# Optimization experiments

Measured on AMD Instinct MI355X. Metric: run time of the kernel, lower is better.

## Reference

```python
import jax, jax.numpy as jnp
import numpy as np

PI = np.pi
NQ = 9  # qubits: edge 0-2, node 3-6 (center=3, neighbor0=4), anc1=7, anc2=8


def _mlp(x, W1, b1, W2, b2):
    h = jax.nn.leaky_relu(x @ W1 + b1, negative_slope=0.2)
    return h @ W2 + b2


def _ry(t):
    h = 0.5 * t
    c = jnp.cos(h).astype(jnp.complex64)
    s = jnp.sin(h).astype(jnp.complex64)
    return jnp.stack([jnp.stack([c, -s]), jnp.stack([s, c])])


def _rx(t):
    h = 0.5 * t
    c = jnp.cos(h).astype(jnp.complex64)
    s = jnp.sin(h).astype(jnp.complex64)
    return jnp.stack([jnp.stack([c, -1j * s]), jnp.stack([-1j * s, c])])


def _rz(t):
    h = (0.5 * t).astype(jnp.complex64)
    e = jnp.exp(-1j * h)
    z = jnp.zeros((), jnp.complex64)
    return jnp.stack([jnp.stack([e, z]), jnp.stack([z, jnp.conj(e)])])


def _ap1(state, U, q):
    s = jnp.moveaxis(state, q, 0)
    s = jnp.tensordot(U, s, axes=([1], [0]))
    return jnp.moveaxis(s, 0, q)


def _apc(state, U, c, t):  # controlled-U, control c, target t
    s = jnp.moveaxis(state, (c, t), (0, 1))
    s1 = jnp.tensordot(U, s[1], axes=([1], [0]))
    s = jnp.stack([s[0], s1])
    return jnp.moveaxis(s, (0, 1), (c, t))


def _cz(state, a, b):
    s = jnp.moveaxis(state, (a, b), (0, 1))
    s = s.at[1, 1].multiply(-1.0)
    return jnp.moveaxis(s, (0, 1), (a, b))


def _pqc(data, theta):
    # data: [18] per-graphlet angles, theta: [27] shared weights; returns <X_center>
    state = jnp.zeros((2,) * NQ, jnp.complex64).at[(0,) * NQ].set(1.0)
    for i in range(3):  # edge qubits: ry, rz
        state = _ap1(state, _ry(data[2 * i]), i)
        state = _ap1(state, _rz(data[2 * i + 1]), i)
    for i in range(4):  # node qubits: ry, rz
        state = _ap1(state, _ry(data[6 + 2 * i]), 3 + i)
        state = _ap1(state, _rz(data[7 + 2 * i]), 3 + i)
    state = _apc(state, _rx(data[14]), 4, 7)  # neighbor -> anc1, c-rx(phi0)
    state = _apc(state, _ry(data[15]), 0, 7)  # edge0    -> anc1, c-ry(phi1)
    state = _apc(state, _rz(data[16]), 4, 8)  # neighbor -> anc2, c-rz(phi2)
    state = _apc(state, _ry(data[17]), 0, 8)  # edge0    -> anc2, c-ry(phi3)
    for b, qs in enumerate([(0, 4, 7), (7, 4, 8), (3, 7, 8)]):  # A, B, U blocks
        th = theta[9 * b:9 * b + 9]
        for i, q in enumerate(qs):
            state = _ap1(state, _rx(th[3 * i + 0]), q)
            state = _ap1(state, _ry(th[3 * i + 1]), q)
            state = _ap1(state, _rz(th[3 * i + 2]), q)
        state = _cz(state, qs[0], qs[1])
        state = _cz(state, qs[1], qs[2])
        state = _cz(state, qs[2], qs[0])
    xs = jnp.moveaxis(jnp.moveaxis(state, 3, 0)[::-1], 0, 3)  # apply X on qubit 3
    return jnp.real(jnp.vdot(state, xs)).astype(jnp.float32)


def setup_inputs() -> dict:
    N, E, K, G = 6000, 96000, 4, 32
    rng = np.random.default_rng(0)
    src = rng.integers(0, N, E)
    dst = (src + 1 + rng.integers(0, N - 1, E)) % N  # no self loops
    pairs = np.stack([np.minimum(src, dst), np.maximum(src, dst)], 1)
    keymap = {(int(u), int(v)): i for i, (u, v) in enumerate(pairs)}
    und = np.unique(np.concatenate([np.stack([src, dst], 1), np.stack([dst, src], 1)], 0), axis=0)
    deg = np.bincount(und[:, 0], minlength=N)
    starts = np.concatenate([[0], np.cumsum(deg)])[:-1]
    gn = np.full((N, K), -1, np.int32)
    gn[:, 0] = np.arange(N)
    ge = np.full((N, K - 1), -1, np.int32)
    for j in range(K - 1):
        has = deg > j
        cs = np.nonzero(has)[0]
        nb = und[starts[has] + j, 1]
        gn[cs, 1 + j] = nb
        for c, n in zip(cs.tolist(), nb.tolist()):
            ge[c, j] = keymap[(min(c, n), max(c, n))]
    batch = ((np.arange(N) * G) // N).astype(np.int32)
    key = jax.random.key(0)
    ks = jax.random.split(key, 12)

    def dense(k, i, o):
        return jax.random.normal(k, (i, o), jnp.float32) / np.sqrt(i)

    return dict(
        node_feat=jax.random.normal(ks[0], (N, 16), jnp.float32),
        edge_attr=jax.random.normal(ks[1], (E, 8), jnp.float32),
        node_W1=dense(ks[2], 16, 128), node_b1=jnp.zeros((128,), jnp.float32),
        node_W2=dense(ks[3], 128, 2), node_b2=jnp.zeros((2,), jnp.float32),
        edge_W1=dense(ks[4], 8, 128), edge_b1=jnp.zeros((128,), jnp.float32),
        edge_W2=dense(ks[5], 128, 2), edge_b2=jnp.zeros((2,), jnp.float32),
        theta=jax.random.uniform(ks[6], (1, 27), jnp.float32, -0.1, 0.1),
        upd_W1=dense(ks[7], 3, 128)[None], upd_b1=jnp.zeros((1, 128), jnp.float32),
        upd_W2=dense(ks[8], 128, 2)[None], upd_b2=jnp.zeros((1, 2), jnp.float32),
        head_W1=dense(ks[9], 2, 2), head_b1=jnp.zeros((2,), jnp.float32),
        head_W2=dense(ks[10], 2, 2), head_b2=jnp.zeros((2,), jnp.float32),
        graphlet_nodes=jnp.asarray(gn), graphlet_edges=jnp.asarray(ge),
        batch=jnp.asarray(batch), num_graphs=G,
    )


def reference(node_feat, edge_attr, node_W1, node_b1, node_W2, node_b2,
              edge_W1, edge_b1, edge_W2, edge_b2, theta,
              upd_W1, upd_b1, upd_W2, upd_b2,
              head_W1, head_b1, head_W2, head_b2,
              graphlet_nodes, graphlet_edges, batch, num_graphs):
    node_f = jnp.tanh(_mlp(node_feat, node_W1, node_b1, node_W2, node_b2)) * PI
    edge_f = jnp.tanh(_mlp(edge_attr, edge_W1, edge_b1, edge_W2, edge_b2)) * PI
    nm = (graphlet_nodes >= 0).astype(node_f.dtype)[..., None]  # pad mask
    em = (graphlet_edges >= 0).astype(edge_f.dtype)[..., None]
    gn = jnp.clip(graphlet_nodes, 0)
    ge = jnp.clip(graphlet_edges, 0)
    N = node_f.shape[0]
    e_feat = edge_f[ge] * em  # [N,3,2] fixed across hops
    for h in range(theta.shape[0]):
        n_feat = node_f[gn] * nm  # [N,4,2]
        phis = jnp.stack([n_feat[:, 1, 0], e_feat[:, 0, 0], n_feat[:, 1, 1], e_feat[:, 0, 1]], 1)
        data = jnp.concatenate([e_feat.reshape(N, 6), n_feat.reshape(N, 8), phis], 1)  # [N,18]
        exp = jax.vmap(_pqc, in_axes=(0, None))(data, theta[h])  # [N]
        upd_inp = jnp.concatenate([node_f[gn[:, 0]], exp[:, None]], 1)  # [N,3]
        upd = _mlp(upd_inp, upd_W1[h], upd_b1[h], upd_W2[h], upd_b2[h])  # [N,2]
        node_f = node_f + jnp.zeros_like(node_f).at[gn[:, 0]].add(upd)
    seg = jax.ops.segment_sum(node_f, batch, num_segments=num_graphs)
    cnt = jax.ops.segment_sum(jnp.ones((N,), node_f.dtype), batch, num_segments=num_graphs)
    emb = seg / cnt[:, None]  # global mean pool
    return _mlp(emb, head_W1, head_b1, head_W2, head_b2)
```

## Files before the change

kernel.cpp:

```cpp
#include <hip/hip_runtime.h>

#define PI_F 3.14159265358979323846f

struct C2 { float r, i; };
struct M2 { C2 m[2][2]; };

__device__ __forceinline__ C2 cmul(C2 a, C2 b){ return C2{a.r*b.r - a.i*b.i, a.r*b.i + a.i*b.r}; }
__device__ __forceinline__ C2 cadd(C2 a, C2 b){ return C2{a.r+b.r, a.i+b.i}; }

__device__ __forceinline__ M2 mmul(M2 A, M2 B){
  M2 R;
  #pragma unroll
  for (int r=0;r<2;++r)
    #pragma unroll
    for (int c=0;c<2;++c)
      R.m[r][c] = cadd(cmul(A.m[r][0],B.m[0][c]), cmul(A.m[r][1],B.m[1][c]));
  return R;
}
__device__ __forceinline__ M2 m_rx(float t){ float s,c; __sincosf(0.5f*t,&s,&c);
  M2 U; U.m[0][0]=C2{c,0}; U.m[0][1]=C2{0,-s}; U.m[1][0]=C2{0,-s}; U.m[1][1]=C2{c,0}; return U; }
__device__ __forceinline__ M2 m_ry(float t){ float s,c; __sincosf(0.5f*t,&s,&c);
  M2 U; U.m[0][0]=C2{c,0}; U.m[0][1]=C2{-s,0}; U.m[1][0]=C2{s,0}; U.m[1][1]=C2{c,0}; return U; }
__device__ __forceinline__ M2 m_rz(float t){ float s,c; __sincosf(0.5f*t,&s,&c);
  M2 U; U.m[0][0]=C2{c,-s}; U.m[0][1]=C2{0,0}; U.m[1][0]=C2{0,0}; U.m[1][1]=C2{c,s}; return U; }
__device__ __forceinline__ M2 fuse_zyx(float tz, float ty, float tx){ return mmul(m_rz(tz), mmul(m_ry(ty), m_rx(tx))); }

__device__ __forceinline__ float fast_tanh(float x){
  float e = __expf(2.f*x);
  return 1.f - 2.f/(e + 1.f);
}

__device__ __forceinline__ M2 selM(bool c, M2 U){
  M2 E;
  E.m[0][0] = c ? U.m[0][0] : C2{1.f,0.f};
  E.m[0][1] = c ? U.m[0][1] : C2{0.f,0.f};
  E.m[1][0] = c ? U.m[1][0] : C2{0.f,0.f};
  E.m[1][1] = c ? U.m[1][1] : C2{1.f,0.f};
  return E;
}

__device__ __forceinline__ M2 loadM(const float* __restrict__ p){
  M2 U;
  U.m[0][0]=C2{p[0],p[1]}; U.m[0][1]=C2{p[2],p[3]};
  U.m[1][0]=C2{p[4],p[5]}; U.m[1][1]=C2{p[6],p[7]};
  return U;
}


template<int STRIDE>
__device__ __forceinline__ void applyReg(M2 U, float (&sr)[8], float (&si)[8]){
  #pragma unroll
  for (int r0=0;r0<8;++r0){
    if (r0 & STRIDE) continue;
    const int r1 = r0 | STRIDE;
    C2 a0{sr[r0], si[r0]}, a1{sr[r1], si[r1]};
    C2 n0 = cadd(cmul(U.m[0][0],a0), cmul(U.m[0][1],a1));
    C2 n1 = cadd(cmul(U.m[1][0],a0), cmul(U.m[1][1],a1));
    sr[r0]=n0.r; si[r0]=n0.i; sr[r1]=n1.r; si[r1]=n1.i;
  }
}

template<int MASK>
__device__ __forceinline__ void applyLane(M2 U, float (&sr)[8], float (&si)[8], int lane){
  const bool b = (lane & MASK) != 0;
  const C2 cs = b ? U.m[1][1] : U.m[0][0];
  const C2 cp = b ? U.m[1][0] : U.m[0][1];
  #pragma unroll
  for (int j=0;j<8;++j){
    float pr  = __shfl_xor(sr[j], MASK);
    float pim = __shfl_xor(si[j], MASK);
    float nr = cs.r*sr[j] - cs.i*si[j] + cp.r*pr  - cp.i*pim;
    float ni = cs.r*si[j] + cs.i*sr[j] + cp.r*pim + cp.i*pr;
    sr[j]=nr; si[j]=ni;
  }
}

__global__ void features_kernel(const float* __restrict__ node_feat,
                                const float* __restrict__ edge_attr,
                                const int* __restrict__ ge,
                                const float* __restrict__ nW1, const float* __restrict__ nb1,
                                const float* __restrict__ nW2, const float* __restrict__ nb2,
                                const float* __restrict__ eW1, const float* __restrict__ eb1,
                                const float* __restrict__ eW2, const float* __restrict__ eb2,
                                float* __restrict__ node_f, float* __restrict__ ef,
                                int N,
                                const float* __restrict__ theta, float* __restrict__ tm){
  const int row = blockIdx.x*blockDim.x + threadIdx.x;
  if (row < 9){
    M2 U = fuse_zyx(theta[3*row+2], theta[3*row+1], theta[3*row+0]);
    float* p = tm + row*8;
    p[0]=U.m[0][0].r; p[1]=U.m[0][0].i;
    p[2]=U.m[0][1].r; p[3]=U.m[0][1].i;
    p[4]=U.m[1][0].r; p[5]=U.m[1][0].i;
    p[6]=U.m[1][1].r; p[7]=U.m[1][1].i;
  }
  if (row < N){
    float xi[16];
    #pragma unroll
    for (int i=0;i<16;++i) xi[i] = node_feat[row*16+i];
    float a0 = nb2[0], a1 = nb2[1];
    #pragma unroll 4
    for (int j=0;j<128;++j){
      float h = nb1[j];
      #pragma unroll
      for (int i=0;i<16;++i) h = fmaf(xi[i], nW1[i*128+j], h);
      h = h > 0.f ? h : 0.2f*h;
      a0 = fmaf(h, nW2[j*2+0], a0);
      a1 = fmaf(h, nW2[j*2+1], a1);
    }
    node_f[row*2+0] = PI_F * fast_tanh(a0);
    node_f[row*2+1] = PI_F * fast_tanh(a1);
  } else {
    const int r = row - N;
    if (r >= 3*N) return;
    const int e = ge[r];
    if (e < 0){ ef[r*2+0] = 0.f; ef[r*2+1] = 0.f; return; }
    float xi[8];
    #pragma unroll
    for (int i=0;i<8;++i) xi[i] = edge_attr[e*8+i];
    float a0 = eb2[0], a1 = eb2[1];
    #pragma unroll 4
    for (int j=0;j<128;++j){
      float h = eb1[j];
      #pragma unroll
      for (int i=0;i<8;++i) h = fmaf(xi[i], eW1[i*128+j], h);
      h = h > 0.f ? h : 0.2f*h;
      a0 = fmaf(h, eW2[j*2+0], a0);
      a1 = fmaf(h, eW2[j*2+1], a1);
    }
    ef[r*2+0] = PI_F * fast_tanh(a0);
    ef[r*2+1] = PI_F * fast_tanh(a1);
  }
}

__global__ void __launch_bounds__(256)
pqc_kernel(const float* __restrict__ node_f, const float* __restrict__ ef,
           const int* __restrict__ gn,
           const float* __restrict__ tm,
           const float* __restrict__ uW1, const float* __restrict__ ub1,
           const float* __restrict__ uW2, const float* __restrict__ ub2,
           float* __restrict__ upd, int N){
  const int lane = threadIdx.x & 63;
  const int n = blockIdx.x*4 + (threadIdx.x >> 6);
  if (n >= N) return;

  float d[18];
  #pragma unroll
  for (int j=0;j<6;++j) d[j] = ef[n*6+j];
  d[6] = node_f[n*2+0];
  d[7] = node_f[n*2+1];
  #pragma unroll
  for (int j=1;j<4;++j){
    int v = gn[n*4+j];
    bool ok = v >= 0; int idx = ok ? v : 0;
    d[6+2*j+0] = ok ? node_f[idx*2+0] : 0.f;
    d[6+2*j+1] = ok ? node_f[idx*2+1] : 0.f;
  }
  d[14]=d[8]; d[15]=d[0]; d[16]=d[9]; d[17]=d[1];

  C2 L{1.f, 0.f};
  {
    auto fold = [&](float ty, float tz, int bit){
      float sy,cy,sz,cz;
      __sincosf(0.5f*ty, &sy, &cy);
      __sincosf(0.5f*tz, &sz, &cz);
      const float amp = bit ? sy : cy;
      const float ph  = bit ? sz : -sz;
      L = cmul(L, C2{amp*cz, amp*ph});
    };
    fold(d[0], d[1], (lane>>5)&1);
    fold(d[2], d[3], (lane>>4)&1);
    fold(d[4], d[5], (lane>>3)&1);
    fold(d[8], d[9], (lane>>2)&1);
    fold(d[10],d[11],(lane>>1)&1);
    fold(d[12],d[13], lane&1);
  }
  float s3y,c3y,s3z,c3z;
  __sincosf(0.5f*d[6], &s3y, &c3y);
  __sincosf(0.5f*d[7], &s3z, &c3z);
  const C2 v30{c3y*c3z, -c3y*s3z}, v31{s3y*c3z, s3y*s3z};

  float sr[8], si[8];
  #pragma unroll
  for (int j=0;j<8;++j){ sr[j]=0.f; si[j]=0.f; }
  { C2 a = cmul(L, v30); sr[0]=a.r; si[0]=a.i; }
  { C2 a = cmul(L, v31); sr[4]=a.r; si[4]=a.i; }

  const bool b4c = (lane & 4)  != 0;
  const bool b0c = (lane & 32) != 0;
  applyReg<2>(mmul(selM(b0c, m_ry(d[15])), selM(b4c, m_rx(d[14]))), sr, si);
  applyReg<1>(mmul(selM(b0c, m_ry(d[17])), selM(b4c, m_rz(d[16]))), sr, si);

  applyLane<32>(loadM(tm+0*8), sr, si, lane);
  applyLane< 4>(loadM(tm+1*8), sr, si, lane);
  applyReg < 2>(loadM(tm+2*8), sr, si);
  {
    const int b0=(lane>>5)&1, b4=(lane>>2)&1;
    const float sA = (b0&b4) ? -1.f : 1.f;
    const float sB = ((b0&b4)^b0^b4) ? -1.f : 1.f;
    #pragma unroll
    for (int r=0;r<8;++r){ const float s = (r&2)? sB : sA; sr[r]*=s; si[r]*=s; }
  }
  applyReg < 2>(loadM(tm+3*8), sr, si);
  applyLane< 4>(loadM(tm+4*8), sr, si, lane);
  applyReg < 1>(loadM(tm+5*8), sr, si);
  {
    const float s4 = (lane & 4) ? -1.f : 1.f;
    #pragma unroll
    for (int r=0;r<8;++r){
      const int b7=(r>>1)&1, b8=r&1;
      if (b7 & b8){ sr[r]=-sr[r]; si[r]=-si[r]; }
      else if (b7 ^ b8){ sr[r]*=s4; si[r]*=s4; }
    }
  }
  applyReg<4>(loadM(tm+6*8), sr, si);
  applyReg<2>(loadM(tm+7*8), sr, si);
  applyReg<1>(loadM(tm+8*8), sr, si);
  {
    #pragma unroll
    for (int r=0;r<8;++r){
      const int b3=(r>>2)&1, b7=(r>>1)&1, b8=r&1;
      if (((b3&b7)^(b7&b8)^(b8&b3)) != 0){ sr[r]=-sr[r]; si[r]=-si[r]; }
    }
  }

  float acc = 0.f;
  #pragma unroll
  for (int r=0;r<8;++r) acc += sr[r]*sr[r^4] + si[r]*si[r^4];
  #pragma unroll
  for (int m=32; m; m>>=1) acc += __shfl_xor(acc, m);

  const float inp0 = d[6];
  const float inp1 = d[7];
  float a0 = 0.f, a1 = 0.f;
  #pragma unroll
  for (int t=0;t<2;++t){
    int j = lane + 64*t;
    float h = ub1[j];
    h = fmaf(inp0, uW1[0*128+j], h);
    h = fmaf(inp1, uW1[1*128+j], h);
    h = fmaf(acc , uW1[2*128+j], h);
    h = h > 0.f ? h : 0.2f*h;
    a0 = fmaf(h, uW2[j*2+0], a0);
    a1 = fmaf(h, uW2[j*2+1], a1);
  }
  #pragma unroll
  for (int m=32; m; m>>=1){ a0 += __shfl_xor(a0, m); a1 += __shfl_xor(a1, m); }

  if (lane==0){
    upd[n*2+0] = a0 + ub2[0];
    upd[n*2+1] = a1 + ub2[1];
  }
}

__global__ void reduce_head_kernel(const float* __restrict__ node_f,
                                   const float* __restrict__ upd,
                                   const float* __restrict__ hW1, const float* __restrict__ hb1,
                                   const float* __restrict__ hW2, const float* __restrict__ hb2,
                                   float* __restrict__ out, int N, int G){
  const int g = blockIdx.x;
  const int start = (g*N + G - 1)/G;
  const int end   = ((g+1)*N + G - 1)/G;
  float a0=0.f, a1=0.f;
  for (int n = start + threadIdx.x; n < end; n += 64){
    a0 += node_f[n*2+0] + upd[n*2+0];
    a1 += node_f[n*2+1] + upd[n*2+1];
  }
  #pragma unroll
  for (int m=32; m; m>>=1){ a0 += __shfl_xor(a0, m); a1 += __shfl_xor(a1, m); }
  if (threadIdx.x == 0){
    const float inv = 1.f / (float)(end - start);
    const float e0 = a0*inv, e1 = a1*inv;
    float h0 = hb1[0] + e0*hW1[0*2+0] + e1*hW1[1*2+0];
    float h1 = hb1[1] + e0*hW1[0*2+1] + e1*hW1[1*2+1];
    h0 = h0 > 0.f ? h0 : 0.2f*h0;
    h1 = h1 > 0.f ? h1 : 0.2f*h1;
    out[g*2+0] = hb2[0] + h0*hW2[0*2+0] + h1*hW2[1*2+0];
    out[g*2+1] = hb2[1] + h0*hW2[0*2+1] + h1*hW2[1*2+1];
  }
}

extern "C" void kernel_launch(void* const* d_in, const int* in_sizes, int n_in,
                              void* d_out, int out_size, void* d_ws, size_t ws_size,
                              hipStream_t stream) {
  const float* node_feat = (const float*)d_in[0];
  const float* edge_attr = (const float*)d_in[1];
  const float* nW1 = (const float*)d_in[2];
  const float* nb1 = (const float*)d_in[3];
  const float* nW2 = (const float*)d_in[4];
  const float* nb2 = (const float*)d_in[5];
  const float* eW1 = (const float*)d_in[6];
  const float* eb1 = (const float*)d_in[7];
  const float* eW2 = (const float*)d_in[8];
  const float* eb2 = (const float*)d_in[9];
  const float* theta = (const float*)d_in[10];
  const float* uW1 = (const float*)d_in[11];
  const float* ub1 = (const float*)d_in[12];
  const float* uW2 = (const float*)d_in[13];
  const float* ub2 = (const float*)d_in[14];
  const float* hW1 = (const float*)d_in[15];
  const float* hb1 = (const float*)d_in[16];
  const float* hW2 = (const float*)d_in[17];
  const float* hb2 = (const float*)d_in[18];
  const int* gn    = (const int*)d_in[19];
  const int* ge    = (const int*)d_in[20];

  const int N = in_sizes[0] / 16;
  const int G = out_size / 2;

  float* node_f = (float*)d_ws;
  float* ef     = node_f + (size_t)N*2;
  float* upd    = ef + (size_t)N*6;
  float* tm     = upd + (size_t)N*2;

  const int R = 4*N;
  features_kernel<<<(R+255)/256, 256, 0, stream>>>(node_feat, edge_attr, ge,
                                                   nW1, nb1, nW2, nb2,
                                                   eW1, eb1, eW2, eb2,
                                                   node_f, ef, N, theta, tm);
  pqc_kernel<<<(N+3)/4, 256, 0, stream>>>(node_f, ef, gn, tm,
                                          uW1, ub1, uW2, ub2, upd, N);
  reduce_head_kernel<<<G, 64, 0, stream>>>(node_f, upd,
                                           hW1, hb1, hW2, hb2, (float*)d_out, N, G);
}
```

Measured before the change: 140.8 us.

## Fuse pooling and head MLP into PQC kernel via last-block atomic counter

Removes the separate reduce_head kernel launch by having each PQC block bump a global atomic counter after a threadfence; the last block to finish does the per-graph mean pool and head MLP. The counter is reset in the features kernel. This saves one launch and its gap, but leaves the whole reduction to a single block with 4 waves looping over all graphs, which could be slower than the previous G-block reduction when N or G is large.

```diff
diff --git a/kernel.cpp b/kernel.cpp
--- a/kernel.cpp
+++ b/kernel.cpp
@@ -84,8 +84,10 @@
                                 const float* __restrict__ eW2, const float* __restrict__ eb2,
                                 float* __restrict__ node_f, float* __restrict__ ef,
                                 int N,
-                                const float* __restrict__ theta, float* __restrict__ tm){
+                                const float* __restrict__ theta, float* __restrict__ tm,
+                                unsigned int* __restrict__ done){
   const int row = blockIdx.x*blockDim.x + threadIdx.x;
+  if (row == 0) *done = 0u;
   if (row < 9){
     M2 U = fuse_zyx(theta[3*row+2], theta[3*row+1], theta[3*row+0]);
     float* p = tm + row*8;
@@ -139,144 +141,156 @@
            const float* __restrict__ tm,
            const float* __restrict__ uW1, const float* __restrict__ ub1,
            const float* __restrict__ uW2, const float* __restrict__ ub2,
-           float* __restrict__ upd, int N){
+           const float* __restrict__ hW1, const float* __restrict__ hb1,
+           const float* __restrict__ hW2, const float* __restrict__ hb2,
+           float* __restrict__ upd, float* __restrict__ out,
+           unsigned int* __restrict__ done,
+           int N, int G){
   const int lane = threadIdx.x & 63;
   const int n = blockIdx.x*4 + (threadIdx.x >> 6);
-  if (n >= N) return;
-
-  float d[18];
-  #pragma unroll
-  for (int j=0;j<6;++j) d[j] = ef[n*6+j];
-  d[6] = node_f[n*2+0];
-  d[7] = node_f[n*2+1];
-  #pragma unroll
-  for (int j=1;j<4;++j){
-    int v = gn[n*4+j];
-    bool ok = v >= 0; int idx = ok ? v : 0;
-    d[6+2*j+0] = ok ? node_f[idx*2+0] : 0.f;
-    d[6+2*j+1] = ok ? node_f[idx*2+1] : 0.f;
-  }
-  d[14]=d[8]; d[15]=d[0]; d[16]=d[9]; d[17]=d[1];
-
-  C2 L{1.f, 0.f};
-  {
-    auto fold = [&](float ty, float tz, int bit){
-      float sy,cy,sz,cz;
-      __sincosf(0.5f*ty, &sy, &cy);
-      __sincosf(0.5f*tz, &sz, &cz);
-      const float amp = bit ? sy : cy;
-      const float ph  = bit ? sz : -sz;
-      L = cmul(L, C2{amp*cz, amp*ph});
-    };
-    fold(d[0], d[1], (lane>>5)&1);
-    fold(d[2], d[3], (lane>>4)&1);
-    fold(d[4], d[5], (lane>>3)&1);
-    fold(d[8], d[9], (lane>>2)&1);
-    fold(d[10],d[11],(lane>>1)&1);
-    fold(d[12],d[13], lane&1);
-  }
-  float s3y,c3y,s3z,c3z;
-  __sincosf(0.5f*d[6], &s3y, &c3y);
-  __sincosf(0.5f*d[7], &s3z, &c3z);
-  const C2 v30{c3y*c3z, -c3y*s3z}, v31{s3y*c3z, s3y*s3z};
-
-  float sr[8], si[8];
-  #pragma unroll
-  for (int j=0;j<8;++j){ sr[j]=0.f; si[j]=0.f; }
-  { C2 a = cmul(L, v30); sr[0]=a.r; si[0]=a.i; }
-  { C2 a = cmul(L, v31); sr[4]=a.r; si[4]=a.i; }
-
-  const bool b4c = (lane & 4)  != 0;
-  const bool b0c = (lane & 32) != 0;
-  applyReg<2>(mmul(selM(b0c, m_ry(d[15])), selM(b4c, m_rx(d[14]))), sr, si);
-  applyReg<1>(mmul(selM(b0c, m_ry(d[17])), selM(b4c, m_rz(d[16]))), sr, si);
-
-  applyLane<32>(loadM(tm+0*8), sr, si, lane);
-  applyLane< 4>(loadM(tm+1*8), sr, si, lane);
-  applyReg < 2>(loadM(tm+2*8), sr, si);
-  {
-    const int b0=(lane>>5)&1, b4=(lane>>2)&1;
-    const float sA = (b0&b4) ? -1.f : 1.f;
-    const float sB = ((b0&b4)^b0^b4) ? -1.f : 1.f;
-    #pragma unroll
-    for (int r=0;r<8;++r){ const float s = (r&2)? sB : sA; sr[r]*=s; si[r]*=s; }
-  }
-  applyReg < 2>(loadM(tm+3*8), sr, si);
-  applyLane< 4>(loadM(tm+4*8), sr, si, lane);
-  applyReg < 1>(loadM(tm+5*8), sr, si);
-  {
-    const float s4 = (lane & 4) ? -1.f : 1.f;
-    #pragma unroll
-    for (int r=0;r<8;++r){
-      const int b7=(r>>1)&1, b8=r&1;
-      if (b7 & b8){ sr[r]=-sr[r]; si[r]=-si[r]; }
-      else if (b7 ^ b8){ sr[r]*=s4; si[r]*=s4; }
-    }
-  }
-  applyReg<4>(loadM(tm+6*8), sr, si);
-  applyReg<2>(loadM(tm+7*8), sr, si);
-  applyReg<1>(loadM(tm+8*8), sr, si);
-  {
-    #pragma unroll
-    for (int r=0;r<8;++r){
-      const int b3=(r>>2)&1, b7=(r>>1)&1, b8=r&1;
-      if (((b3&b7)^(b7&b8)^(b8&b3)) != 0){ sr[r]=-sr[r]; si[r]=-si[r]; }
-    }
-  }
-
-  float acc = 0.f;
-  #pragma unroll
-  for (int r=0;r<8;++r) acc += sr[r]*sr[r^4] + si[r]*si[r^4];
-  #pragma unroll
-  for (int m=32; m; m>>=1) acc += __shfl_xor(acc, m);
-
-  const float inp0 = d[6];
-  const float inp1 = d[7];
-  float a0 = 0.f, a1 = 0.f;
-  #pragma unroll
-  for (int t=0;t<2;++t){
-    int j = lane + 64*t;
-    float h = ub1[j];
-    h = fmaf(inp0, uW1[0*128+j], h);
-    h = fmaf(inp1, uW1[1*128+j], h);
-    h = fmaf(acc , uW1[2*128+j], h);
-    h = h > 0.f ? h : 0.2f*h;
-    a0 = fmaf(h, uW2[j*2+0], a0);
-    a1 = fmaf(h, uW2[j*2+1], a1);
-  }
-  #pragma unroll
-  for (int m=32; m; m>>=1){ a0 += __shfl_xor(a0, m); a1 += __shfl_xor(a1, m); }
-
-  if (lane==0){
-    upd[n*2+0] = a0 + ub2[0];
-    upd[n*2+1] = a1 + ub2[1];
-  }
-}
-
-__global__ void reduce_head_kernel(const float* __restrict__ node_f,
-                                   const float* __restrict__ upd,
-                                   const float* __restrict__ hW1, const float* __restrict__ hb1,
-                                   const float* __restrict__ hW2, const float* __restrict__ hb2,
-                                   float* __restrict__ out, int N, int G){
-  const int g = blockIdx.x;
-  const int start = (g*N + G - 1)/G;
-  const int end   = ((g+1)*N + G - 1)/G;
-  float a0=0.f, a1=0.f;
-  for (int n = start + threadIdx.x; n < end; n += 64){
-    a0 += node_f[n*2+0] + upd[n*2+0];
-    a1 += node_f[n*2+1] + upd[n*2+1];
-  }
-  #pragma unroll
-  for (int m=32; m; m>>=1){ a0 += __shfl_xor(a0, m); a1 += __shfl_xor(a1, m); }
+
+  if (n < N){
+    float d[18];
+    #pragma unroll
+    for (int j=0;j<6;++j) d[j] = ef[n*6+j];
+    d[6] = node_f[n*2+0];
+    d[7] = node_f[n*2+1];
+    #pragma unroll
+    for (int j=1;j<4;++j){
+      int v = gn[n*4+j];
+      bool ok = v >= 0; int idx = ok ? v : 0;
+      d[6+2*j+0] = ok ? node_f[idx*2+0] : 0.f;
+      d[6+2*j+1] = ok ? node_f[idx*2+1] : 0.f;
+    }
+    d[14]=d[8]; d[15]=d[0]; d[16]=d[9]; d[17]=d[1];
+
+    C2 L{1.f, 0.f};
+    {
+      auto fold = [&](float ty, float tz, int bit){
+        float sy,cy,sz,cz;
+        __sincosf(0.5f*ty, &sy, &cy);
+        __sincosf(0.5f*tz, &sz, &cz);
+        const float amp = bit ? sy : cy;
+        const float ph  = bit ? sz : -sz;
+        L = cmul(L, C2{amp*cz, amp*ph});
+      };
+      fold(d[0], d[1], (lane>>5)&1);
+      fold(d[2], d[3], (lane>>4)&1);
+      fold(d[4], d[5], (lane>>3)&1);
+      fold(d[8], d[9], (lane>>2)&1);
+      fold(d[10],d[11],(lane>>1)&1);
+      fold(d[12],d[13], lane&1);
+    }
+    float s3y,c3y,s3z,c3z;
+    __sincosf(0.5f*d[6], &s3y, &c3y);
+    __sincosf(0.5f*d[7], &s3z, &c3z);
+    const C2 v30{c3y*c3z, -c3y*s3z}, v31{s3y*c3z, s3y*s3z};
+
+    float sr[8], si[8];
+    #pragma unroll
+    for (int j=0;j<8;++j){ sr[j]=0.f; si[j]=0.f; }
+    { C2 a = cmul(L, v30); sr[0]=a.r; si[0]=a.i; }
+    { C2 a = cmul(L, v31); sr[4]=a.r; si[4]=a.i; }
+
+    const bool b4c = (lane & 4)  != 0;
+    const bool b0c = (lane & 32) != 0;
+    applyReg<2>(mmul(selM(b0c, m_ry(d[15])), selM(b4c, m_rx(d[14]))), sr, si);
+    applyReg<1>(mmul(selM(b0c, m_ry(d[17])), selM(b4c, m_rz(d[16]))), sr, si);
+
+    applyLane<32>(loadM(tm+0*8), sr, si, lane);
+    applyLane< 4>(loadM(tm+1*8), sr, si, lane);
+    applyReg < 2>(loadM(tm+2*8), sr, si);
+    {
+      const int b0=(lane>>5)&1, b4=(lane>>2)&1;
+      const float sA = (b0&b4) ? -1.f : 1.f;
+      const float sB = ((b0&b4)^b0^b4) ? -1.f : 1.f;
+      #pragma unroll
+      for (int r=0;r<8;++r){ const float s = (r&2)? sB : sA; sr[r]*=s; si[r]*=s; }
+    }
+    applyReg < 2>(loadM(tm+3*8), sr, si);
+    applyLane< 4>(loadM(tm+4*8), sr, si, lane);
+    applyReg < 1>(loadM(tm+5*8), sr, si);
+    {
+      const float s4 = (lane & 4) ? -1.f : 1.f;
+      #pragma unroll
+      for (int r=0;r<8;++r){
+        const int b7=(r>>1)&1, b8=r&1;
+        if (b7 & b8){ sr[r]=-sr[r]; si[r]=-si[r]; }
+        else if (b7 ^ b8){ sr[r]*=s4; si[r]*=s4; }
+      }
+    }
+    applyReg<4>(loadM(tm+6*8), sr, si);
+    applyReg<2>(loadM(tm+7*8), sr, si);
+    applyReg<1>(loadM(tm+8*8), sr, si);
+    {
+      #pragma unroll
+      for (int r=0;r<8;++r){
+        const int b3=(r>>2)&1, b7=(r>>1)&1, b8=r&1;
+        if (((b3&b7)^(b7&b8)^(b8&b3)) != 0){ sr[r]=-sr[r]; si[r]=-si[r]; }
+      }
+    }
+
+    float acc = 0.f;
+    #pragma unroll
+    for (int r=0;r<8;++r) acc += sr[r]*sr[r^4] + si[r]*si[r^4];
+    #pragma unroll
+    for (int m=32; m; m>>=1) acc += __shfl_xor(acc, m);
+
+    const float inp0 = d[6];
+    const float inp1 = d[7];
+    float a0 = 0.f, a1 = 0.f;
+    #pragma unroll
+    for (int t=0;t<2;++t){
+      int j = lane + 64*t;
+      float h = ub1[j];
+      h = fmaf(inp0, uW1[0*128+j], h);
+      h = fmaf(inp1, uW1[1*128+j], h);
+      h = fmaf(acc , uW1[2*128+j], h);
+      h = h > 0.f ? h : 0.2f*h;
+      a0 = fmaf(h, uW2[j*2+0], a0);
+      a1 = fmaf(h, uW2[j*2+1], a1);
+    }
+    #pragma unroll
+    for (int m=32; m; m>>=1){ a0 += __shfl_xor(a0, m); a1 += __shfl_xor(a1, m); }
+
+    if (lane==0){
+      upd[n*2+0] = a0 + ub2[0];
+      upd[n*2+1] = a1 + ub2[1];
+    }
+  }
+
+  __shared__ bool amLast;
+  __threadfence();
+  __syncthreads();
   if (threadIdx.x == 0){
-    const float inv = 1.f / (float)(end - start);
-    const float e0 = a0*inv, e1 = a1*inv;
-    float h0 = hb1[0] + e0*hW1[0*2+0] + e1*hW1[1*2+0];
-    float h1 = hb1[1] + e0*hW1[0*2+1] + e1*hW1[1*2+1];
-    h0 = h0 > 0.f ? h0 : 0.2f*h0;
-    h1 = h1 > 0.f ? h1 : 0.2f*h1;
-    out[g*2+0] = hb2[0] + h0*hW2[0*2+0] + h1*hW2[1*2+0];
-    out[g*2+1] = hb2[1] + h0*hW2[0*2+1] + h1*hW2[1*2+1];
+    unsigned int old = atomicAdd(done, 1u);
+    amLast = (old == gridDim.x - 1);
+  }
+  __syncthreads();
+  if (!amLast) return;
+  __threadfence();
+
+  const int w = threadIdx.x >> 6;
+  for (int g = w; g < G; g += 4){
+    const int start = (g*N + G - 1)/G;
+    const int end   = ((g+1)*N + G - 1)/G;
+    float a0=0.f, a1=0.f;
+    for (int nn = start + lane; nn < end; nn += 64){
+      a0 += node_f[nn*2+0] + upd[nn*2+0];
+      a1 += node_f[nn*2+1] + upd[nn*2+1];
+    }
+    #pragma unroll
+    for (int m=32; m; m>>=1){ a0 += __shfl_xor(a0, m); a1 += __shfl_xor(a1, m); }
+    if (lane == 0){
+      const float inv = 1.f / (float)(end - start);
+      const float e0 = a0*inv, e1 = a1*inv;
+      float h0 = hb1[0] + e0*hW1[0*2+0] + e1*hW1[1*2+0];
+      float h1 = hb1[1] + e0*hW1[0*2+1] + e1*hW1[1*2+1];
+      h0 = h0 > 0.f ? h0 : 0.2f*h0;
+      h1 = h1 > 0.f ? h1 : 0.2f*h1;
+      out[g*2+0] = hb2[0] + h0*hW2[0*2+0] + h1*hW2[1*2+0];
+      out[g*2+1] = hb2[1] + h0*hW2[0*2+1] + h1*hW2[1*2+1];
+    }
   }
 }
 
@@ -312,14 +326,15 @@
   float* ef     = node_f + (size_t)N*2;
   float* upd    = ef + (size_t)N*6;
   float* tm     = upd + (size_t)N*2;
+  unsigned int* done = (unsigned int*)(tm + 80);
 
   const int R = 4*N;
   features_kernel<<<(R+255)/256, 256, 0, stream>>>(node_feat, edge_attr, ge,
                                                    nW1, nb1, nW2, nb2,
                                                    eW1, eb1, eW2, eb2,
-                                                   node_f, ef, N, theta, tm);
+                                                   node_f, ef, N, theta, tm, done);
   pqc_kernel<<<(N+3)/4, 256, 0, stream>>>(node_f, ef, gn, tm,
-                                          uW1, ub1, uW2, ub2, upd, N);
-  reduce_head_kernel<<<G, 64, 0, stream>>>(node_f, upd,
-                                           hW1, hb1, hW2, hb2, (float*)d_out, N, G);
-}
+                                          uW1, ub1, uW2, ub2,
+                                          hW1, hb1, hW2, hb2,
+                                          upd, (float*)d_out, done, N, G);
+}
```

Result: slower. 234.4 us (+66.4%).

## Process two graphlets per wavefront in PQC kernel to amortize shuffles and loads

Applied to the files above, without the earlier changes.

Each wavefront now simulates two graphlets at once, holding 16 complex amplitudes per lane instead of 8. Gate matrices, the MLP weights and the shuffle setup are shared across both. The aim is more independent work per lane for instruction-level parallelism, fewer waves, and half as many redundant weight loads. The cost is higher register pressure (launch bounds set to 256,2) and possible loss of occupancy. The final output is written as a single float4 store.

```diff
diff --git a/kernel.cpp b/kernel.cpp
--- a/kernel.cpp
+++ b/kernel.cpp
@@ -48,11 +48,12 @@
 
 
 template<int STRIDE>
-__device__ __forceinline__ void applyReg(M2 U, float (&sr)[8], float (&si)[8]){
-  #pragma unroll
-  for (int r0=0;r0<8;++r0){
+__device__ __forceinline__ void applyReg2(M2 U0, M2 U1, float (&sr)[16], float (&si)[16]){
+  #pragma unroll
+  for (int r0=0;r0<16;++r0){
     if (r0 & STRIDE) continue;
     const int r1 = r0 | STRIDE;
+    const M2& U = (r0 < 8) ? U0 : U1;
     C2 a0{sr[r0], si[r0]}, a1{sr[r1], si[r1]};
     C2 n0 = cadd(cmul(U.m[0][0],a0), cmul(U.m[0][1],a1));
     C2 n1 = cadd(cmul(U.m[1][0],a0), cmul(U.m[1][1],a1));
@@ -61,18 +62,65 @@
 }
 
 template<int MASK>
-__device__ __forceinline__ void applyLane(M2 U, float (&sr)[8], float (&si)[8], int lane){
+__device__ __forceinline__ void applyLane2(M2 U0, M2 U1, float (&sr)[16], float (&si)[16], int lane){
   const bool b = (lane & MASK) != 0;
-  const C2 cs = b ? U.m[1][1] : U.m[0][0];
-  const C2 cp = b ? U.m[1][0] : U.m[0][1];
-  #pragma unroll
-  for (int j=0;j<8;++j){
+  const C2 cs0 = b ? U0.m[1][1] : U0.m[0][0];
+  const C2 cp0 = b ? U0.m[1][0] : U0.m[0][1];
+  const C2 cs1 = b ? U1.m[1][1] : U1.m[0][0];
+  const C2 cp1 = b ? U1.m[1][0] : U1.m[0][1];
+  #pragma unroll
+  for (int j=0;j<16;++j){
+    const C2 cs = (j < 8) ? cs0 : cs1;
+    const C2 cp = (j < 8) ? cp0 : cp1;
     float pr  = __shfl_xor(sr[j], MASK);
     float pim = __shfl_xor(si[j], MASK);
     float nr = cs.r*sr[j] - cs.i*si[j] + cp.r*pr  - cp.i*pim;
     float ni = cs.r*si[j] + cs.i*sr[j] + cp.r*pim + cp.i*pr;
     sr[j]=nr; si[j]=ni;
   }
+}
+
+__device__ __forceinline__ void gatherD(const float* __restrict__ node_f,
+                                        const float* __restrict__ ef,
+                                        const int* __restrict__ gn,
+                                        int n, float (&d)[18]){
+  #pragma unroll
+  for (int j=0;j<6;++j) d[j] = ef[n*6+j];
+  d[6] = node_f[n*2+0];
+  d[7] = node_f[n*2+1];
+  #pragma unroll
+  for (int j=1;j<4;++j){
+    int v = gn[n*4+j];
+    bool ok = v >= 0; int idx = ok ? v : 0;
+    d[6+2*j+0] = ok ? node_f[idx*2+0] : 0.f;
+    d[6+2*j+1] = ok ? node_f[idx*2+1] : 0.f;
+  }
+  d[14]=d[8]; d[15]=d[0]; d[16]=d[9]; d[17]=d[1];
+}
+
+__device__ __forceinline__ void initState(const float (&d)[18], int lane, int s,
+                                          float (&sr)[16], float (&si)[16]){
+  C2 L{1.f, 0.f};
+  auto fold = [&](float ty, float tz, int bit){
+    float sy,cy,sz,cz;
+    __sincosf(0.5f*ty, &sy, &cy);
+    __sincosf(0.5f*tz, &sz, &cz);
+    const float amp = bit ? sy : cy;
+    const float ph  = bit ? sz : -sz;
+    L = cmul(L, C2{amp*cz, amp*ph});
+  };
+  fold(d[0], d[1], (lane>>5)&1);
+  fold(d[2], d[3], (lane>>4)&1);
+  fold(d[4], d[5], (lane>>3)&1);
+  fold(d[8], d[9], (lane>>2)&1);
+  fold(d[10],d[11],(lane>>1)&1);
+  fold(d[12],d[13], lane&1);
+  float s3y,c3y,s3z,c3z;
+  __sincosf(0.5f*d[6], &s3y, &c3y);
+  __sincosf(0.5f*d[7], &s3z, &c3z);
+  const C2 v30{c3y*c3z, -c3y*s3z}, v31{s3y*c3z, s3y*s3z};
+  C2 a = cmul(L, v30); sr[s*8+0]=a.r; si[s*8+0]=a.i;
+  C2 b = cmul(L, v31); sr[s*8+4]=b.r; si[s*8+4]=b.i;
 }
 
 __global__ void features_kernel(const float* __restrict__ node_feat,
@@ -133,7 +181,7 @@
   }
 }
 
-__global__ void __launch_bounds__(256)
+__global__ void __launch_bounds__(256, 2)
 pqc_kernel(const float* __restrict__ node_f, const float* __restrict__ ef,
            const int* __restrict__ gn,
            const float* __restrict__ tm,
@@ -141,115 +189,99 @@
            const float* __restrict__ uW2, const float* __restrict__ ub2,
            float* __restrict__ upd, int N){
   const int lane = threadIdx.x & 63;
-  const int n = blockIdx.x*4 + (threadIdx.x >> 6);
-  if (n >= N) return;
-
-  float d[18];
-  #pragma unroll
-  for (int j=0;j<6;++j) d[j] = ef[n*6+j];
-  d[6] = node_f[n*2+0];
-  d[7] = node_f[n*2+1];
-  #pragma unroll
-  for (int j=1;j<4;++j){
-    int v = gn[n*4+j];
-    bool ok = v >= 0; int idx = ok ? v : 0;
-    d[6+2*j+0] = ok ? node_f[idx*2+0] : 0.f;
-    d[6+2*j+1] = ok ? node_f[idx*2+1] : 0.f;
-  }
-  d[14]=d[8]; d[15]=d[0]; d[16]=d[9]; d[17]=d[1];
-
-  C2 L{1.f, 0.f};
-  {
-    auto fold = [&](float ty, float tz, int bit){
-      float sy,cy,sz,cz;
-      __sincosf(0.5f*ty, &sy, &cy);
-      __sincosf(0.5f*tz, &sz, &cz);
-      const float amp = bit ? sy : cy;
-      const float ph  = bit ? sz : -sz;
-      L = cmul(L, C2{amp*cz, amp*ph});
-    };
-    fold(d[0], d[1], (lane>>5)&1);
-    fold(d[2], d[3], (lane>>4)&1);
-    fold(d[4], d[5], (lane>>3)&1);
-    fold(d[8], d[9], (lane>>2)&1);
-    fold(d[10],d[11],(lane>>1)&1);
-    fold(d[12],d[13], lane&1);
-  }
-  float s3y,c3y,s3z,c3z;
-  __sincosf(0.5f*d[6], &s3y, &c3y);
-  __sincosf(0.5f*d[7], &s3z, &c3z);
-  const C2 v30{c3y*c3z, -c3y*s3z}, v31{s3y*c3z, s3y*s3z};
-
-  float sr[8], si[8];
-  #pragma unroll
-  for (int j=0;j<8;++j){ sr[j]=0.f; si[j]=0.f; }
-  { C2 a = cmul(L, v30); sr[0]=a.r; si[0]=a.i; }
-  { C2 a = cmul(L, v31); sr[4]=a.r; si[4]=a.i; }
+  const int base = (blockIdx.x*4 + (threadIdx.x >> 6)) * 2;
+  if (base >= N) return;
+  const int n0 = base;
+  const int n1 = (base+1 < N) ? base+1 : base;
+
+  float d0[18], d1[18];
+  gatherD(node_f, ef, gn, n0, d0);
+  gatherD(node_f, ef, gn, n1, d1);
+
+  float sr[16], si[16];
+  #pragma unroll
+  for (int j=0;j<16;++j){ sr[j]=0.f; si[j]=0.f; }
+  initState(d0, lane, 0, sr, si);
+  initState(d1, lane, 1, sr, si);
 
   const bool b4c = (lane & 4)  != 0;
   const bool b0c = (lane & 32) != 0;
-  applyReg<2>(mmul(selM(b0c, m_ry(d[15])), selM(b4c, m_rx(d[14]))), sr, si);
-  applyReg<1>(mmul(selM(b0c, m_ry(d[17])), selM(b4c, m_rz(d[16]))), sr, si);
-
-  applyLane<32>(loadM(tm+0*8), sr, si, lane);
-  applyLane< 4>(loadM(tm+1*8), sr, si, lane);
-  applyReg < 2>(loadM(tm+2*8), sr, si);
+  applyReg2<2>(mmul(selM(b0c, m_ry(d0[15])), selM(b4c, m_rx(d0[14]))),
+               mmul(selM(b0c, m_ry(d1[15])), selM(b4c, m_rx(d1[14]))), sr, si);
+  applyReg2<1>(mmul(selM(b0c, m_ry(d0[17])), selM(b4c, m_rz(d0[16]))),
+               mmul(selM(b0c, m_ry(d1[17])), selM(b4c, m_rz(d1[16]))), sr, si);
+
+  { M2 U = loadM(tm+0*8); applyLane2<32>(U, U, sr, si, lane); }
+  { M2 U = loadM(tm+1*8); applyLane2< 4>(U, U, sr, si, lane); }
+  { M2 U = loadM(tm+2*8); applyReg2 < 2>(U, U, sr, si);       }
   {
     const int b0=(lane>>5)&1, b4=(lane>>2)&1;
     const float sA = (b0&b4) ? -1.f : 1.f;
     const float sB = ((b0&b4)^b0^b4) ? -1.f : 1.f;
     #pragma unroll
-    for (int r=0;r<8;++r){ const float s = (r&2)? sB : sA; sr[r]*=s; si[r]*=s; }
-  }
-  applyReg < 2>(loadM(tm+3*8), sr, si);
-  applyLane< 4>(loadM(tm+4*8), sr, si, lane);
-  applyReg < 1>(loadM(tm+5*8), sr, si);
+    for (int r=0;r<16;++r){ const float s = (r&2)? sB : sA; sr[r]*=s; si[r]*=s; }
+  }
+  { M2 U = loadM(tm+3*8); applyReg2 < 2>(U, U, sr, si);       }
+  { M2 U = loadM(tm+4*8); applyLane2< 4>(U, U, sr, si, lane); }
+  { M2 U = loadM(tm+5*8); applyReg2 < 1>(U, U, sr, si);       }
   {
     const float s4 = (lane & 4) ? -1.f : 1.f;
     #pragma unroll
-    for (int r=0;r<8;++r){
+    for (int r=0;r<16;++r){
       const int b7=(r>>1)&1, b8=r&1;
       if (b7 & b8){ sr[r]=-sr[r]; si[r]=-si[r]; }
       else if (b7 ^ b8){ sr[r]*=s4; si[r]*=s4; }
     }
   }
-  applyReg<4>(loadM(tm+6*8), sr, si);
-  applyReg<2>(loadM(tm+7*8), sr, si);
-  applyReg<1>(loadM(tm+8*8), sr, si);
+  { M2 U = loadM(tm+6*8); applyReg2<4>(U, U, sr, si); }
+  { M2 U = loadM(tm+7*8); applyReg2<2>(U, U, sr, si); }
+  { M2 U = loadM(tm+8*8); applyReg2<1>(U, U, sr, si); }
   {
     #pragma unroll
-    for (int r=0;r<8;++r){
+    for (int r=0;r<16;++r){
       const int b3=(r>>2)&1, b7=(r>>1)&1, b8=r&1;
       if (((b3&b7)^(b7&b8)^(b8&b3)) != 0){ sr[r]=-sr[r]; si[r]=-si[r]; }
     }
   }
 
-  float acc = 0.f;
-  #pragma unroll
-  for (int r=0;r<8;++r) acc += sr[r]*sr[r^4] + si[r]*si[r^4];
-  #pragma unroll
-  for (int m=32; m; m>>=1) acc += __shfl_xor(acc, m);
-
-  const float inp0 = d[6];
-  const float inp1 = d[7];
-  float a0 = 0.f, a1 = 0.f;
+  float acc0 = 0.f, acc1 = 0.f;
+  #pragma unroll
+  for (int r=0;r<16;++r){
+    const float v = sr[r]*sr[r^4] + si[r]*si[r^4];
+    if (r < 8) acc0 += v; else acc1 += v;
+  }
+  #pragma unroll
+  for (int m=32; m; m>>=1){ acc0 += __shfl_xor(acc0, m); acc1 += __shfl_xor(acc1, m); }
+
+  float a00=0.f, a01=0.f, a10=0.f, a11=0.f;
   #pragma unroll
   for (int t=0;t<2;++t){
     int j = lane + 64*t;
-    float h = ub1[j];
-    h = fmaf(inp0, uW1[0*128+j], h);
-    h = fmaf(inp1, uW1[1*128+j], h);
-    h = fmaf(acc , uW1[2*128+j], h);
-    h = h > 0.f ? h : 0.2f*h;
-    a0 = fmaf(h, uW2[j*2+0], a0);
-    a1 = fmaf(h, uW2[j*2+1], a1);
-  }
-  #pragma unroll
-  for (int m=32; m; m>>=1){ a0 += __shfl_xor(a0, m); a1 += __shfl_xor(a1, m); }
+    const float w0 = uW1[0*128+j], w1 = uW1[1*128+j], w2 = uW1[2*128+j], bb = ub1[j];
+    const float v0 = uW2[j*2+0],  v1 = uW2[j*2+1];
+    float h0 = bb;
+    h0 = fmaf(d0[6], w0, h0); h0 = fmaf(d0[7], w1, h0); h0 = fmaf(acc0, w2, h0);
+    h0 = h0 > 0.f ? h0 : 0.2f*h0;
+    float h1 = bb;
+    h1 = fmaf(d1[6], w0, h1); h1 = fmaf(d1[7], w1, h1); h1 = fmaf(acc1, w2, h1);
+    h1 = h1 > 0.f ? h1 : 0.2f*h1;
+    a00 = fmaf(h0, v0, a00); a01 = fmaf(h0, v1, a01);
+    a10 = fmaf(h1, v0, a10); a11 = fmaf(h1, v1, a11);
+  }
+  #pragma unroll
+  for (int m=32; m; m>>=1){
+    a00 += __shfl_xor(a00, m); a01 += __shfl_xor(a01, m);
+    a10 += __shfl_xor(a10, m); a11 += __shfl_xor(a11, m);
+  }
 
   if (lane==0){
-    upd[n*2+0] = a0 + ub2[0];
-    upd[n*2+1] = a1 + ub2[1];
+    if (base+1 < N){
+      float4 o = make_float4(a00 + ub2[0], a01 + ub2[1], a10 + ub2[0], a11 + ub2[1]);
+      *(float4*)&upd[base*2] = o;
+    } else {
+      upd[base*2+0] = a00 + ub2[0];
+      upd[base*2+1] = a01 + ub2[1];
+    }
   }
 }
 
@@ -318,7 +350,7 @@
                                                    nW1, nb1, nW2, nb2,
                                                    eW1, eb1, eW2, eb2,
                                                    node_f, ef, N, theta, tm);
-  pqc_kernel<<<(N+3)/4, 256, 0, stream>>>(node_f, ef, gn, tm,
+  pqc_kernel<<<(N+7)/8, 256, 0, stream>>>(node_f, ef, gn, tm,
                                           uW1, ub1, uW2, ub2, upd, N);
   reduce_head_kernel<<<G, 64, 0, stream>>>(node_f, upd,
                                            hW1, hb1, hW2, hb2, (float*)d_out, N, G);
```

After: 137.9 us. 2.1% less time.

## Reduce PQC to 5-qubit light cone, one thread per graphlet

Applied to the files above, without the earlier changes.

Drops the qubits that cannot affect <X_center> (edge qubits 1-2 and node qubits 5-6), leaving a 32-amplitude state per graphlet held in registers of a single thread instead of spread across a 64-lane wavefront with shuffles. Only the first edge is passed through the edge MLP, which cuts that part of the feature kernel's work by a factor of three. The update MLP now runs serially per thread over 128 hidden units instead of being split across lanes with a reduction. In exchange there is higher register pressure (64 floats of state), fewer waves per node count, and a longer serial MLP loop per thread.

```diff
diff --git a/kernel.cpp b/kernel.cpp
--- a/kernel.cpp
+++ b/kernel.cpp
@@ -30,15 +30,6 @@
   return 1.f - 2.f/(e + 1.f);
 }
 
-__device__ __forceinline__ M2 selM(bool c, M2 U){
-  M2 E;
-  E.m[0][0] = c ? U.m[0][0] : C2{1.f,0.f};
-  E.m[0][1] = c ? U.m[0][1] : C2{0.f,0.f};
-  E.m[1][0] = c ? U.m[1][0] : C2{0.f,0.f};
-  E.m[1][1] = c ? U.m[1][1] : C2{1.f,0.f};
-  return E;
-}
-
 __device__ __forceinline__ M2 loadM(const float* __restrict__ p){
   M2 U;
   U.m[0][0]=C2{p[0],p[1]}; U.m[0][1]=C2{p[2],p[3]};
@@ -47,31 +38,25 @@
 }
 
 
-template<int STRIDE>
-__device__ __forceinline__ void applyReg(M2 U, float (&sr)[8], float (&si)[8]){
-  #pragma unroll
-  for (int r0=0;r0<8;++r0){
-    if (r0 & STRIDE) continue;
-    const int r1 = r0 | STRIDE;
-    C2 a0{sr[r0], si[r0]}, a1{sr[r1], si[r1]};
-    C2 n0 = cadd(cmul(U.m[0][0],a0), cmul(U.m[0][1],a1));
-    C2 n1 = cadd(cmul(U.m[1][0],a0), cmul(U.m[1][1],a1));
-    sr[r0]=n0.r; si[r0]=n0.i; sr[r1]=n1.r; si[r1]=n1.i;
-  }
-}
-
-template<int MASK>
-__device__ __forceinline__ void applyLane(M2 U, float (&sr)[8], float (&si)[8], int lane){
-  const bool b = (lane & MASK) != 0;
-  const C2 cs = b ? U.m[1][1] : U.m[0][0];
-  const C2 cp = b ? U.m[1][0] : U.m[0][1];
-  #pragma unroll
-  for (int j=0;j<8;++j){
-    float pr  = __shfl_xor(sr[j], MASK);
-    float pim = __shfl_xor(si[j], MASK);
-    float nr = cs.r*sr[j] - cs.i*si[j] + cp.r*pr  - cp.i*pim;
-    float ni = cs.r*si[j] + cs.i*sr[j] + cp.r*pim + cp.i*pr;
-    sr[j]=nr; si[j]=ni;
+template<int T>
+__device__ __forceinline__ void applyT(M2 U, float (&sr)[32], float (&si)[32]){
+  #pragma unroll
+  for (int a0=0;a0<32;++a0){
+    if (a0 & T) continue;
+    const int a1 = a0 | T;
+    C2 x0{sr[a0], si[a0]}, x1{sr[a1], si[a1]};
+    C2 n0 = cadd(cmul(U.m[0][0],x0), cmul(U.m[0][1],x1));
+    C2 n1 = cadd(cmul(U.m[1][0],x0), cmul(U.m[1][1],x1));
+    sr[a0]=n0.r; si[a0]=n0.i; sr[a1]=n1.r; si[a1]=n1.i;
+  }
+}
+
+template<int BA,int BB,int BC>
+__device__ __forceinline__ void czTriple(float (&sr)[32], float (&si)[32]){
+  #pragma unroll
+  for (int a=0;a<32;++a){
+    const int x=(a&BA)?1:0, y=(a&BB)?1:0, z=(a&BC)?1:0;
+    if (((x&y)^(y&z)^(z&x)) != 0){ sr[a]=-sr[a]; si[a]=-si[a]; }
   }
 }
 
@@ -112,8 +97,8 @@
     node_f[row*2+1] = PI_F * fast_tanh(a1);
   } else {
     const int r = row - N;
-    if (r >= 3*N) return;
-    const int e = ge[r];
+    if (r >= N) return;
+    const int e = ge[r*3+0];
     if (e < 0){ ef[r*2+0] = 0.f; ef[r*2+1] = 0.f; return; }
     float xi[8];
     #pragma unroll
@@ -133,124 +118,111 @@
   }
 }
 
-__global__ void __launch_bounds__(256)
+__global__ void __launch_bounds__(64, 1)
 pqc_kernel(const float* __restrict__ node_f, const float* __restrict__ ef,
            const int* __restrict__ gn,
            const float* __restrict__ tm,
            const float* __restrict__ uW1, const float* __restrict__ ub1,
            const float* __restrict__ uW2, const float* __restrict__ ub2,
            float* __restrict__ upd, int N){
-  const int lane = threadIdx.x & 63;
-  const int n = blockIdx.x*4 + (threadIdx.x >> 6);
+  const int n = blockIdx.x*64 + threadIdx.x;
   if (n >= N) return;
 
-  float d[18];
-  #pragma unroll
-  for (int j=0;j<6;++j) d[j] = ef[n*6+j];
-  d[6] = node_f[n*2+0];
-  d[7] = node_f[n*2+1];
-  #pragma unroll
-  for (int j=1;j<4;++j){
-    int v = gn[n*4+j];
-    bool ok = v >= 0; int idx = ok ? v : 0;
-    d[6+2*j+0] = ok ? node_f[idx*2+0] : 0.f;
-    d[6+2*j+1] = ok ? node_f[idx*2+1] : 0.f;
-  }
-  d[14]=d[8]; d[15]=d[0]; d[16]=d[9]; d[17]=d[1];
-
-  C2 L{1.f, 0.f};
-  {
-    auto fold = [&](float ty, float tz, int bit){
-      float sy,cy,sz,cz;
-      __sincosf(0.5f*ty, &sy, &cy);
-      __sincosf(0.5f*tz, &sz, &cz);
-      const float amp = bit ? sy : cy;
-      const float ph  = bit ? sz : -sz;
-      L = cmul(L, C2{amp*cz, amp*ph});
-    };
-    fold(d[0], d[1], (lane>>5)&1);
-    fold(d[2], d[3], (lane>>4)&1);
-    fold(d[4], d[5], (lane>>3)&1);
-    fold(d[8], d[9], (lane>>2)&1);
-    fold(d[10],d[11],(lane>>1)&1);
-    fold(d[12],d[13], lane&1);
-  }
-  float s3y,c3y,s3z,c3z;
-  __sincosf(0.5f*d[6], &s3y, &c3y);
-  __sincosf(0.5f*d[7], &s3z, &c3z);
-  const C2 v30{c3y*c3z, -c3y*s3z}, v31{s3y*c3z, s3y*s3z};
-
-  float sr[8], si[8];
-  #pragma unroll
-  for (int j=0;j<8;++j){ sr[j]=0.f; si[j]=0.f; }
-  { C2 a = cmul(L, v30); sr[0]=a.r; si[0]=a.i; }
-  { C2 a = cmul(L, v31); sr[4]=a.r; si[4]=a.i; }
-
-  const bool b4c = (lane & 4)  != 0;
-  const bool b0c = (lane & 32) != 0;
-  applyReg<2>(mmul(selM(b0c, m_ry(d[15])), selM(b4c, m_rx(d[14]))), sr, si);
-  applyReg<1>(mmul(selM(b0c, m_ry(d[17])), selM(b4c, m_rz(d[16]))), sr, si);
-
-  applyLane<32>(loadM(tm+0*8), sr, si, lane);
-  applyLane< 4>(loadM(tm+1*8), sr, si, lane);
-  applyReg < 2>(loadM(tm+2*8), sr, si);
-  {
-    const int b0=(lane>>5)&1, b4=(lane>>2)&1;
-    const float sA = (b0&b4) ? -1.f : 1.f;
-    const float sB = ((b0&b4)^b0^b4) ? -1.f : 1.f;
-    #pragma unroll
-    for (int r=0;r<8;++r){ const float s = (r&2)? sB : sA; sr[r]*=s; si[r]*=s; }
-  }
-  applyReg < 2>(loadM(tm+3*8), sr, si);
-  applyLane< 4>(loadM(tm+4*8), sr, si, lane);
-  applyReg < 1>(loadM(tm+5*8), sr, si);
-  {
-    const float s4 = (lane & 4) ? -1.f : 1.f;
-    #pragma unroll
-    for (int r=0;r<8;++r){
-      const int b7=(r>>1)&1, b8=r&1;
-      if (b7 & b8){ sr[r]=-sr[r]; si[r]=-si[r]; }
-      else if (b7 ^ b8){ sr[r]*=s4; si[r]*=s4; }
+  const float e0 = ef[n*2+0], e1 = ef[n*2+1];
+  const float f0 = node_f[n*2+0], f1 = node_f[n*2+1];
+  const int v1 = gn[n*4+1];
+  const bool ok = v1 >= 0; const int idx = ok ? v1 : 0;
+  const float g0 = ok ? node_f[idx*2+0] : 0.f;
+  const float g1 = ok ? node_f[idx*2+1] : 0.f;
+
+  float sy0,cy0,sz0,cz0, sy3,cy3,sz3,cz3, sy4,cy4,sz4,cz4;
+  __sincosf(0.5f*e0,&sy0,&cy0); __sincosf(0.5f*e1,&sz0,&cz0);
+  __sincosf(0.5f*f0,&sy3,&cy3); __sincosf(0.5f*f1,&sz3,&cz3);
+  __sincosf(0.5f*g0,&sy4,&cy4); __sincosf(0.5f*g1,&sz4,&cz4);
+
+  const C2 v0[2] = { C2{cy0*cz0, -cy0*sz0}, C2{sy0*cz0, sy0*sz0} };
+  const C2 v3[2] = { C2{cy3*cz3, -cy3*sz3}, C2{sy3*cz3, sy3*sz3} };
+  const C2 v4[2] = { C2{cy4*cz4, -cy4*sz4}, C2{sy4*cz4, sy4*sz4} };
+
+  float sr[32], si[32];
+  #pragma unroll
+  for (int a=0;a<32;++a){ sr[a]=0.f; si[a]=0.f; }
+  #pragma unroll
+  for (int b4=0;b4<2;++b4){
+    #pragma unroll
+    for (int b3=0;b3<2;++b3){
+      const C2 t = cmul(v0[b4], v3[b3]);
+      #pragma unroll
+      for (int b2=0;b2<2;++b2){
+        const C2 a = cmul(t, v4[b2]);
+        const int ix = b4*16 + b3*8 + b2*4;
+        sr[ix]=a.r; si[ix]=a.i;
+      }
     }
   }
-  applyReg<4>(loadM(tm+6*8), sr, si);
-  applyReg<2>(loadM(tm+7*8), sr, si);
-  applyReg<1>(loadM(tm+8*8), sr, si);
-  {
-    #pragma unroll
-    for (int r=0;r<8;++r){
-      const int b3=(r>>2)&1, b7=(r>>1)&1, b8=r&1;
-      if (((b3&b7)^(b7&b8)^(b8&b3)) != 0){ sr[r]=-sr[r]; si[r]=-si[r]; }
-    }
-  }
+
+  #pragma unroll
+  for (int a0=0;a0<32;++a0){
+    if ((a0 & 2) || !(a0 & 4)) continue;
+    const int a1 = a0 | 2;
+    const float r0=sr[a0], i0=si[a0], r1=sr[a1], i1=si[a1];
+    sr[a0] = cy4*r0 + sy4*i1;  si[a0] = cy4*i0 - sy4*r1;
+    sr[a1] = sy4*i0 + cy4*r1;  si[a1] = -sy4*r0 + cy4*i1;
+  }
+  #pragma unroll
+  for (int a0=0;a0<32;++a0){
+    if ((a0 & 2) || !(a0 & 16)) continue;
+    const int a1 = a0 | 2;
+    const float r0=sr[a0], i0=si[a0], r1=sr[a1], i1=si[a1];
+    sr[a0] = cy0*r0 - sy0*r1;  si[a0] = cy0*i0 - sy0*i1;
+    sr[a1] = sy0*r0 + cy0*r1;  si[a1] = sy0*i0 + cy0*i1;
+  }
+  #pragma unroll
+  for (int a=0;a<32;++a){
+    if (!(a & 4)) continue;
+    const float r=sr[a], im=si[a];
+    if (a & 1){ sr[a] = r*cz4 - im*sz4;  si[a] = im*cz4 + r*sz4; }
+    else      { sr[a] = r*cz4 + im*sz4;  si[a] = im*cz4 - r*sz4; }
+  }
+  #pragma unroll
+  for (int a0=0;a0<32;++a0){
+    if ((a0 & 1) || !(a0 & 16)) continue;
+    const int a1 = a0 | 1;
+    const float r0=sr[a0], i0=si[a0], r1=sr[a1], i1=si[a1];
+    sr[a0] = cz0*r0 - sz0*r1;  si[a0] = cz0*i0 - sz0*i1;
+    sr[a1] = sz0*r0 + cz0*r1;  si[a1] = sz0*i0 + cz0*i1;
+  }
+
+  applyT<16>(loadM(tm+0*8), sr, si);
+  applyT< 4>(loadM(tm+1*8), sr, si);
+  applyT< 2>(loadM(tm+2*8), sr, si);
+  czTriple<16,4,2>(sr, si);
+  applyT< 2>(loadM(tm+3*8), sr, si);
+  applyT< 4>(loadM(tm+4*8), sr, si);
+  applyT< 1>(loadM(tm+5*8), sr, si);
+  czTriple<2,4,1>(sr, si);
+  applyT< 8>(loadM(tm+6*8), sr, si);
+  applyT< 2>(loadM(tm+7*8), sr, si);
+  applyT< 1>(loadM(tm+8*8), sr, si);
+  czTriple<8,2,1>(sr, si);
 
   float acc = 0.f;
   #pragma unroll
-  for (int r=0;r<8;++r) acc += sr[r]*sr[r^4] + si[r]*si[r^4];
-  #pragma unroll
-  for (int m=32; m; m>>=1) acc += __shfl_xor(acc, m);
-
-  const float inp0 = d[6];
-  const float inp1 = d[7];
-  float a0 = 0.f, a1 = 0.f;
-  #pragma unroll
-  for (int t=0;t<2;++t){
-    int j = lane + 64*t;
+  for (int a=0;a<32;++a) acc += sr[a]*sr[a^8] + si[a]*si[a^8];
+
+  float o0 = ub2[0], o1 = ub2[1];
+  #pragma unroll 4
+  for (int j=0;j<128;++j){
     float h = ub1[j];
-    h = fmaf(inp0, uW1[0*128+j], h);
-    h = fmaf(inp1, uW1[1*128+j], h);
-    h = fmaf(acc , uW1[2*128+j], h);
+    h = fmaf(f0,  uW1[0*128+j], h);
+    h = fmaf(f1,  uW1[1*128+j], h);
+    h = fmaf(acc, uW1[2*128+j], h);
     h = h > 0.f ? h : 0.2f*h;
-    a0 = fmaf(h, uW2[j*2+0], a0);
-    a1 = fmaf(h, uW2[j*2+1], a1);
-  }
-  #pragma unroll
-  for (int m=32; m; m>>=1){ a0 += __shfl_xor(a0, m); a1 += __shfl_xor(a1, m); }
-
-  if (lane==0){
-    upd[n*2+0] = a0 + ub2[0];
-    upd[n*2+1] = a1 + ub2[1];
-  }
+    o0 = fmaf(h, uW2[j*2+0], o0);
+    o1 = fmaf(h, uW2[j*2+1], o1);
+  }
+  upd[n*2+0] = o0;
+  upd[n*2+1] = o1;
 }
 
 __global__ void reduce_head_kernel(const float* __restrict__ node_f,
@@ -310,16 +282,16 @@
 
   float* node_f = (float*)d_ws;
   float* ef     = node_f + (size_t)N*2;
-  float* upd    = ef + (size_t)N*6;
+  float* upd    = ef + (size_t)N*2;
   float* tm     = upd + (size_t)N*2;
 
-  const int R = 4*N;
+  const int R = 2*N;
   features_kernel<<<(R+255)/256, 256, 0, stream>>>(node_feat, edge_attr, ge,
                                                    nW1, nb1, nW2, nb2,
                                                    eW1, eb1, eW2, eb2,
                                                    node_f, ef, N, theta, tm);
-  pqc_kernel<<<(N+3)/4, 256, 0, stream>>>(node_f, ef, gn, tm,
-                                          uW1, ub1, uW2, ub2, upd, N);
+  pqc_kernel<<<(N+63)/64, 64, 0, stream>>>(node_f, ef, gn, tm,
+                                           uW1, ub1, uW2, ub2, upd, N);
   reduce_head_kernel<<<G, 64, 0, stream>>>(node_f, upd,
                                            hW1, hb1, hW2, hb2, (float*)d_out, N, G);
 }
```

Measured after the change: 141.2 us. No clear change (+0.3%).
